# Optimization experiments

Hardware: AMD Instinct MI355X
Metric: run time of the kernel (lower is better)

Reference implementation:

```python
import jax, jax.numpy as jnp
import numpy as np

FEAT_DIM = 2048
HID = 256
N = 1024
NUM_CLASSES = 16
BN_EPS = 1e-5


def _batchnorm(x, gamma, beta):
    # training-mode BatchNorm1d: per-batch mean, biased variance
    m = x.mean(axis=0)
    v = x.var(axis=0)
    return gamma * (x - m) / jnp.sqrt(v + BN_EPS) + beta


def setup_inputs() -> dict:
    key = jax.random.key(0)
    ks = jax.random.split(key, 12)
    s1 = 1.0 / np.sqrt(FEAT_DIM)
    s2 = 1.0 / np.sqrt(HID)
    s3 = 1.0 / np.sqrt(2 * HID)
    return {
        "features": jax.random.normal(ks[0], (N, FEAT_DIM), dtype=jnp.float32),
        "labels": jax.random.randint(ks[1], (N,), 0, NUM_CLASSES, dtype=jnp.int32),
        # semantic disentangler
        "W1": jax.random.normal(ks[2], (FEAT_DIM, HID), dtype=jnp.float32) * s1,
        "b1": jnp.zeros((HID,), jnp.float32),
        "g1": jnp.ones((HID,), jnp.float32),
        "bt1": jnp.zeros((HID,), jnp.float32),
        "W2": jax.random.normal(ks[3], (HID, HID), dtype=jnp.float32) * s2,
        "b2": jnp.zeros((HID,), jnp.float32),
        "g2": jnp.ones((HID,), jnp.float32),
        "bt2": jnp.zeros((HID,), jnp.float32),
        # edge network: Linear(2H -> H), Linear(H -> 1)
        "We1": jax.random.normal(ks[4], (2 * HID, HID), dtype=jnp.float32) * s3,
        "bwe1": jnp.zeros((HID,), jnp.float32),
        "We2": jax.random.normal(ks[5], (HID, 1), dtype=jnp.float32) * s2,
        "bwe2": jnp.zeros((1,), jnp.float32),
    }


def reference(features, labels, W1, b1, g1, bt1, W2, b2, g2, bt2,
              We1, bwe1, We2, bwe2):
    # semantic disentangler: (Linear -> BN -> ReLU) x2
    h = jax.nn.relu(_batchnorm(features @ W1 + b1, g1, bt1))
    di = jax.nn.relu(_batchnorm(h @ W2 + b2, g2, bt2))  # [N, H]

    # EdgeNetwork all-pairs: Linear on concat([f_i, f_j]) splits into two GEMMs
    hi = di @ We1[:HID]   # [N, H] contribution of node i (first half of concat)
    hj = di @ We1[HID:]   # [N, H] contribution of node j (second half)
    pair = jax.nn.relu(hi[:, None, :] + hj[None, :, :] + bwe1)  # [N, N, H]
    logits = pair @ We2[:, 0] + bwe2[0]                          # [N, N]
    same_label = labels[:, None] == labels[None, :]
    off_diag = ~jnp.eye(N, dtype=bool)
    edge_weights = jnp.where(same_label & off_diag,
                             jax.nn.sigmoid(logits), 0.0)        # [N, N]

    # update_node_features: f_i + sum_j w_ij f_j / sum_j w_ij (if wsum > 0)
    weighted_sum = edge_weights @ di                 # [N, H] (w_ii == 0)
    wsum = edge_weights.sum(axis=1, keepdims=True)   # [N, 1]
    denom = jnp.where(wsum > 0, wsum, 1.0)
    updated = di + jnp.where(wsum > 0, weighted_sum / denom, 0.0)
    return updated
```

## Files before the change

kernel.cpp:

```cpp
#include <hip/hip_runtime.h>
#include <math.h>

#define N_PTS 1024
#define HID   256
#define FEAT  2048

typedef short bf16x8 __attribute__((ext_vector_type(8)));
typedef float f32x4  __attribute__((ext_vector_type(4)));

__device__ inline ushort f2bf(float f) {
    union { float f; unsigned u; } v; v.f = f;
    unsigned r = v.u + 0x7fff + ((v.u >> 16) & 1);
    return (ushort)(r >> 16);
}

__global__ __launch_bounds__(256) void prep(
    const float* __restrict__ features, const float* __restrict__ W1,
    const float* __restrict__ W2, const float* __restrict__ We1,
    ushort* __restrict__ Af, ushort* __restrict__ W1T,
    ushort* __restrict__ W2T, ushort* __restrict__ WeT)
{
    const int tid = threadIdx.x;
    int b = blockIdx.x;
    if (b < 512) {
        #pragma unroll
        for (int q = 0; q < 2; q++) {
            const size_t g = (size_t)b * 256 + tid + (size_t)q * 131072;
            float4 v0 = ((const float4*)features)[g * 2];
            float4 v1 = ((const float4*)features)[g * 2 + 1];
            bf16x8 o;
            o[0] = (short)f2bf(v0.x); o[1] = (short)f2bf(v0.y);
            o[2] = (short)f2bf(v0.z); o[3] = (short)f2bf(v0.w);
            o[4] = (short)f2bf(v1.x); o[5] = (short)f2bf(v1.y);
            o[6] = (short)f2bf(v1.z); o[7] = (short)f2bf(v1.w);
            ((bf16x8*)Af)[g] = o;
        }
        return;
    }
    __shared__ ushort Ts[64 * 72];
    const float* src; ushort* dst; int K;
    b -= 512;
    if (b < 128)      { src = W1;  dst = W1T; K = 2048; }
    else if (b < 144) { b -= 128; src = W2;  dst = W2T; K = 256; }
    else              { b -= 144; src = We1; dst = WeT; K = 512; }
    const int k0 = (b >> 2) * 64;
    const int n0 = (b & 3) * 64;
    #pragma unroll
    for (int p = 0; p < 4; p++) {
        const int c  = p * 256 + tid;
        const int r  = c >> 4;
        const int cq = c & 15;
        float4 v = *(const float4*)&src[(size_t)(k0 + r) * 256 + n0 + cq * 4];
        Ts[(cq * 4 + 0) * 72 + r] = f2bf(v.x);
        Ts[(cq * 4 + 1) * 72 + r] = f2bf(v.y);
        Ts[(cq * 4 + 2) * 72 + r] = f2bf(v.z);
        Ts[(cq * 4 + 3) * 72 + r] = f2bf(v.w);
    }
    __syncthreads();
    #pragma unroll
    for (int p = 0; p < 2; p++) {
        const int c    = p * 256 + tid;
        const int row  = c >> 3;
        const int col8 = c & 7;
        *(bf16x8*)&dst[(size_t)(n0 + row) * K + k0 + col8 * 8] =
            *(bf16x8*)&Ts[row * 72 + col8 * 8];
    }
}

__global__ __launch_bounds__(256) void gemm_bf(
    const ushort* __restrict__ A, const ushort* __restrict__ B,
    float* __restrict__ C, int lda, int ldb, int ldc, int kchunk)
{
    __shared__ ushort As[64 * 72];
    __shared__ ushort Bs[64 * 72];
    const int tid  = threadIdx.x;
    const int lane = tid & 63;
    const int wave = tid >> 6;
    const int wy = wave >> 1, wx = wave & 1;
    const int quad = lane >> 4, l16 = lane & 15;
    const int mBase = blockIdx.y * 64;
    const int nBase = blockIdx.x * 64;
    const int kBeg  = blockIdx.z * kchunk;

    f32x4 acc[2][2] = {};
    for (int ks = kBeg; ks < kBeg + kchunk; ks += 64) {
        #pragma unroll
        for (int p = 0; p < 2; p++) {
            const int c    = p * 256 + tid;
            const int row  = c >> 3;
            const int col8 = c & 7;
            *(bf16x8*)&As[row * 72 + col8 * 8] =
                *(const bf16x8*)&A[(size_t)(mBase + row) * lda + ks + col8 * 8];
            *(bf16x8*)&Bs[row * 72 + col8 * 8] =
                *(const bf16x8*)&B[(size_t)(nBase + row) * ldb + ks + col8 * 8];
        }
        __syncthreads();
        #pragma unroll
        for (int kt = 0; kt < 64; kt += 32) {
            bf16x8 af[2], bfr[2];
            #pragma unroll
            for (int mi = 0; mi < 2; mi++)
                af[mi] = *(bf16x8*)&As[(wy * 32 + mi * 16 + l16) * 72 + kt + quad * 8];
            #pragma unroll
            for (int ni = 0; ni < 2; ni++)
                bfr[ni] = *(bf16x8*)&Bs[(wx * 32 + ni * 16 + l16) * 72 + kt + quad * 8];
            #pragma unroll
            for (int mi = 0; mi < 2; mi++)
                #pragma unroll
                for (int ni = 0; ni < 2; ni++)
                    acc[mi][ni] = __builtin_amdgcn_mfma_f32_16x16x32_bf16(
                        af[mi], bfr[ni], acc[mi][ni], 0, 0, 0);
        }
        __syncthreads();
    }
    #pragma unroll
    for (int mi = 0; mi < 2; mi++)
        #pragma unroll
        for (int ni = 0; ni < 2; ni++)
            #pragma unroll
            for (int e = 0; e < 4; e++) {
                const int gm = mBase + wy * 32 + mi * 16 + quad * 4 + e;
                const int gn = nBase + wx * 32 + ni * 16 + l16;
                unsafeAtomicAdd(&C[(size_t)gm * ldc + gn], acc[mi][ni][e]);
            }
}

__global__ __launch_bounds__(256) void colstats(
    const float* __restrict__ X, float* __restrict__ sum,
    float* __restrict__ sq, int rowsPerBlock)
{
    const int c = threadIdx.x;
    const int r0 = blockIdx.x * rowsPerBlock;
    float s = 0.f, q = 0.f;
    for (int r = r0; r < r0 + rowsPerBlock; ++r) {
        float v = X[r * HID + c];
        s += v;
        q = fmaf(v, v, q);
    }
    unsafeAtomicAdd(&sum[c], s);
    unsafeAtomicAdd(&sq[c], q);
}

__global__ __launch_bounds__(256) void gemm2_fused(
    const float* __restrict__ A , const ushort* __restrict__ B ,
    float* __restrict__ C ,
    const float* __restrict__ sum1, const float* __restrict__ sq1,
    const float* __restrict__ g1, const float* __restrict__ bt1,
    float* __restrict__ sum2, float* __restrict__ sq2)
{
    __shared__ ushort As[64 * 72];
    __shared__ ushort Bs[64 * 72];
    __shared__ float sscale[HID];
    __shared__ float sshift[HID];
    __shared__ float csum[64];
    __shared__ float csq[64];
    const int tid  = threadIdx.x;
    const int lane = tid & 63;
    const int wave = tid >> 6;
    const int wy = wave >> 1, wx = wave & 1;
    const int quad = lane >> 4, l16 = lane & 15;
    const int mBase = blockIdx.y * 64;
    const int nBase = blockIdx.x * 64;

    {
        float m   = sum1[tid] * (1.f / 1024.f);
        float var = fmaf(-m, m, sq1[tid] * (1.f / 1024.f));
        float rstd = rsqrtf(var + 1e-5f);
        float sc = g1[tid] * rstd;
        sscale[tid] = sc;
        sshift[tid] = fmaf(-m, sc, bt1[tid]);
    }
    if (tid < 64) { csum[tid] = 0.f; csq[tid] = 0.f; }
    __syncthreads();

    f32x4 acc[2][2] = {};
    for (int ks = 0; ks < HID; ks += 64) {
        #pragma unroll
        for (int p = 0; p < 4; p++) {
            const int c  = p * 256 + tid;
            const int r  = c >> 4;
            const int cq = c & 15;
            const int k0 = ks + cq * 4;
            float4 av = *(const float4*)&A[(size_t)(mBase + r) * HID + k0];
            float v0 = fmaxf(fmaf(sscale[k0 + 0], av.x, sshift[k0 + 0]), 0.f);
            float v1 = fmaxf(fmaf(sscale[k0 + 1], av.y, sshift[k0 + 1]), 0.f);
            float v2 = fmaxf(fmaf(sscale[k0 + 2], av.z, sshift[k0 + 2]), 0.f);
            float v3 = fmaxf(fmaf(sscale[k0 + 3], av.w, sshift[k0 + 3]), 0.f);
            ushort4 ao;
            ao.x = f2bf(v0); ao.y = f2bf(v1); ao.z = f2bf(v2); ao.w = f2bf(v3);
            *(ushort4*)&As[r * 72 + cq * 4] = ao;
        }
        #pragma unroll
        for (int p = 0; p < 2; p++) {
            const int c    = p * 256 + tid;
            const int row  = c >> 3;
            const int col8 = c & 7;
            *(bf16x8*)&Bs[row * 72 + col8 * 8] =
                *(const bf16x8*)&B[(size_t)(nBase + row) * HID + ks + col8 * 8];
        }
        __syncthreads();
        #pragma unroll
        for (int kt = 0; kt < 64; kt += 32) {
            bf16x8 af[2], bfr[2];
            #pragma unroll
            for (int mi = 0; mi < 2; mi++)
                af[mi] = *(bf16x8*)&As[(wy * 32 + mi * 16 + l16) * 72 + kt + quad * 8];
            #pragma unroll
            for (int ni = 0; ni < 2; ni++)
                bfr[ni] = *(bf16x8*)&Bs[(wx * 32 + ni * 16 + l16) * 72 + kt + quad * 8];
            #pragma unroll
            for (int mi = 0; mi < 2; mi++)
                #pragma unroll
                for (int ni = 0; ni < 2; ni++)
                    acc[mi][ni] = __builtin_amdgcn_mfma_f32_16x16x32_bf16(
                        af[mi], bfr[ni], acc[mi][ni], 0, 0, 0);
        }
        __syncthreads();
    }

    float s[2] = {0.f, 0.f}, q[2] = {0.f, 0.f};
    #pragma unroll
    for (int mi = 0; mi < 2; mi++)
        #pragma unroll
        for (int ni = 0; ni < 2; ni++)
            #pragma unroll
            for (int e = 0; e < 4; e++) {
                const int gm = mBase + wy * 32 + mi * 16 + quad * 4 + e;
                const int gn = nBase + wx * 32 + ni * 16 + l16;
                float v = acc[mi][ni][e];
                C[(size_t)gm * HID + gn] = v;
                s[ni] += v;
                q[ni] = fmaf(v, v, q[ni]);
            }
    #pragma unroll
    for (int ni = 0; ni < 2; ni++) {
        float sv = s[ni], qv = q[ni];
        sv += __shfl_xor(sv, 16, 64); sv += __shfl_xor(sv, 32, 64);
        qv += __shfl_xor(qv, 16, 64); qv += __shfl_xor(qv, 32, 64);
        if (quad == 0) {
            atomicAdd(&csum[wx * 32 + ni * 16 + l16], sv);
            atomicAdd(&csq [wx * 32 + ni * 16 + l16], qv);
        }
    }
    __syncthreads();
    if (tid < 64) {
        unsafeAtomicAdd(&sum2[nBase + tid], csum[tid]);
        unsafeAtomicAdd(&sq2 [nBase + tid], csq[tid]);
    }
}

__global__ __launch_bounds__(256) void gemm_dual_bn(
    const float* __restrict__ A , const ushort* __restrict__ WeT,
    float* __restrict__ C1 , float* __restrict__ C2 ,
    const float* __restrict__ sum2, const float* __restrict__ sq2,
    const float* __restrict__ g2, const float* __restrict__ bt2,
    float* __restrict__ di)
{
    __shared__ ushort As[64 * 72];
    __shared__ ushort Bs[64 * 72];
    __shared__ float sscale[HID];
    __shared__ float sshift[HID];
    const int tid  = threadIdx.x;
    const int lane = tid & 63;
    const int wave = tid >> 6;
    const int wy = wave >> 1, wx = wave & 1;
    const int quad = lane >> 4, l16 = lane & 15;
    const int mBase = blockIdx.y * 64;
    const int nBase = blockIdx.x * 64;
    const int half  = blockIdx.z >> 2;
    const int ks    = (blockIdx.z & 3) * 64;
    float* C = half ? C2 : C1;
    const bool writeDi = (blockIdx.x == 0) && (half == 0);

    {
        float m   = sum2[tid] * (1.f / 1024.f);
        float var = fmaf(-m, m, sq2[tid] * (1.f / 1024.f));
        float rstd = rsqrtf(var + 1e-5f);
        float sc = g2[tid] * rstd;
        sscale[tid] = sc;
        sshift[tid] = fmaf(-m, sc, bt2[tid]);
    }
    __syncthreads();

    #pragma unroll
    for (int p = 0; p < 4; p++) {
        const int c  = p * 256 + tid;
        const int r  = c >> 4;
        const int cq = c & 15;
        const int k0 = ks + cq * 4;
        float4 av = *(const float4*)&A[(size_t)(mBase + r) * HID + k0];
        float v0 = fmaxf(fmaf(sscale[k0 + 0], av.x, sshift[k0 + 0]), 0.f);
        float v1 = fmaxf(fmaf(sscale[k0 + 1], av.y, sshift[k0 + 1]), 0.f);
        float v2 = fmaxf(fmaf(sscale[k0 + 2], av.z, sshift[k0 + 2]), 0.f);
        float v3 = fmaxf(fmaf(sscale[k0 + 3], av.w, sshift[k0 + 3]), 0.f);
        if (writeDi)
            *(float4*)&di[(size_t)(mBase + r) * HID + k0] =
                make_float4(v0, v1, v2, v3);
        ushort4 ao;
        ao.x = f2bf(v0); ao.y = f2bf(v1); ao.z = f2bf(v2); ao.w = f2bf(v3);
        *(ushort4*)&As[r * 72 + cq * 4] = ao;
    }
    #pragma unroll
    for (int p = 0; p < 2; p++) {
        const int c    = p * 256 + tid;
        const int row  = c >> 3;
        const int col8 = c & 7;
        *(bf16x8*)&Bs[row * 72 + col8 * 8] =
            *(const bf16x8*)&WeT[(size_t)(nBase + row) * 512 + half * 256 + ks + col8 * 8];
    }
    __syncthreads();

    f32x4 acc[2][2] = {};
    #pragma unroll
    for (int kt = 0; kt < 64; kt += 32) {
        bf16x8 af[2], bfr[2];
        #pragma unroll
        for (int mi = 0; mi < 2; mi++)
            af[mi] = *(bf16x8*)&As[(wy * 32 + mi * 16 + l16) * 72 + kt + quad * 8];
        #pragma unroll
        for (int ni = 0; ni < 2; ni++)
            bfr[ni] = *(bf16x8*)&Bs[(wx * 32 + ni * 16 + l16) * 72 + kt + quad * 8];
        #pragma unroll
        for (int mi = 0; mi < 2; mi++)
            #pragma unroll
            for (int ni = 0; ni < 2; ni++)
                acc[mi][ni] = __builtin_amdgcn_mfma_f32_16x16x32_bf16(
                    af[mi], bfr[ni], acc[mi][ni], 0, 0, 0);
    }
    #pragma unroll
    for (int mi = 0; mi < 2; mi++)
        #pragma unroll
        for (int ni = 0; ni < 2; ni++)
            #pragma unroll
            for (int e = 0; e < 4; e++) {
                const int gm = mBase + wy * 32 + mi * 16 + quad * 4 + e;
                const int gn = nBase + wx * 32 + ni * 16 + l16;
                unsafeAtomicAdd(&C[(size_t)gm * HID + gn], acc[mi][ni][e]);
            }
}

__global__ __launch_bounds__(256) void pair_update2(
    const float* __restrict__ di, const float* __restrict__ hi,
    const float* __restrict__ hj, const float* __restrict__ bwe1,
    const float* __restrict__ We2, const float* __restrict__ bwe2,
    const int* __restrict__ labels, float* __restrict__ out)
{
    __shared__ int   slab[N_PTS];
    __shared__ int   list[N_PTS];
    __shared__ int   cnt;
    __shared__ float sacc[16][HID];
    __shared__ float swsum[16];
    const int i   = blockIdx.x;
    const int tid = threadIdx.x;
    const int pid = tid >> 4;
    const int l16 = tid & 15;

    if (tid == 0) cnt = 0;
    for (int t = tid; t < N_PTS; t += 256) slab[t] = labels[t];
    __syncthreads();
    const int myLab = slab[i];
    for (int t = tid; t < N_PTS; t += 256)
        if (slab[t] == myLab && t != i) list[atomicAdd(&cnt, 1)] = t;
    __syncthreads();
    const int n = cnt;

    const float4* hip4 = (const float4*)(hi + (size_t)i * HID) + l16 * 4;
    const float4* bw4  = (const float4*)bwe1 + l16 * 4;
    const float4* w24  = (const float4*)We2  + l16 * 4;
    float4 hb[4], w2[4];
    #pragma unroll
    for (int s = 0; s < 4; s++) {
        float4 a = hip4[s], b = bw4[s];
        hb[s] = make_float4(a.x + b.x, a.y + b.y, a.z + b.z, a.w + b.w);
        w2[s] = w24[s];
    }
    const float b2 = bwe2[0];

    float4 acc[4] = {};
    float wloc = 0.f;
    const int rounds = (n + 15) >> 4;
    for (int r = 0; r < rounds; ++r) {
        const int idx = r * 16 + pid;
        const bool valid = idx < n;
        const int jj = valid ? list[idx] : i;
        const float4* hv4 = (const float4*)(hj + (size_t)jj * HID) + l16 * 4;
        float4 hv[4];
        #pragma unroll
        for (int s = 0; s < 4; s++) hv[s] = hv4[s];
        float p = 0.f;
        #pragma unroll
        for (int s = 0; s < 4; s++) {
            p = fmaf(fmaxf(hb[s].x + hv[s].x, 0.f), w2[s].x, p);
            p = fmaf(fmaxf(hb[s].y + hv[s].y, 0.f), w2[s].y, p);
            p = fmaf(fmaxf(hb[s].z + hv[s].z, 0.f), w2[s].z, p);
            p = fmaf(fmaxf(hb[s].w + hv[s].w, 0.f), w2[s].w, p);
        }
        p += __shfl_xor(p, 1, 64);
        p += __shfl_xor(p, 2, 64);
        p += __shfl_xor(p, 4, 64);
        p += __shfl_xor(p, 8, 64);
        const float w = valid ? 1.f / (1.f + expf(-(p + b2))) : 0.f;
        const float4* dv4 = (const float4*)(di + (size_t)jj * HID) + l16 * 4;
        #pragma unroll
        for (int s = 0; s < 4; s++) {
            float4 d = dv4[s];
            acc[s].x = fmaf(w, d.x, acc[s].x);
            acc[s].y = fmaf(w, d.y, acc[s].y);
            acc[s].z = fmaf(w, d.z, acc[s].z);
            acc[s].w = fmaf(w, d.w, acc[s].w);
        }
        if (l16 == 0) wloc += w;
    }
    #pragma unroll
    for (int s = 0; s < 4; s++)
        ((float4*)&sacc[pid][l16 * 16])[s] = acc[s];
    if (l16 == 0) swsum[pid] = wloc;
    __syncthreads();

    float at = 0.f;
    #pragma unroll
    for (int g = 0; g < 16; g++) at += sacc[g][tid];
    float wt = 0.f;
    #pragma unroll
    for (int g = 0; g < 16; g++) wt += swsum[g];
    const float dval = di[(size_t)i * HID + tid];
    out[(size_t)i * HID + tid] = dval + (wt > 0.f ? at / wt : 0.f);
}

extern "C" void kernel_launch(void* const* d_in, const int* in_sizes, int n_in,
                              void* d_out, int out_size, void* d_ws, size_t ws_size,
                              hipStream_t stream)
{
    const float* features = (const float*)d_in[0];
    const int*   labels   = (const int*)d_in[1];
    const float* W1   = (const float*)d_in[2];
    const float* g1   = (const float*)d_in[4];
    const float* bt1  = (const float*)d_in[5];
    const float* W2   = (const float*)d_in[6];
    const float* g2   = (const float*)d_in[8];
    const float* bt2  = (const float*)d_in[9];
    const float* We1  = (const float*)d_in[10];
    const float* bwe1 = (const float*)d_in[11];
    const float* We2  = (const float*)d_in[12];
    const float* bwe2 = (const float*)d_in[13];
    float* out = (float*)d_out;

    float* ws    = (float*)d_ws;
    float* x1    = ws;
    float* hi    = ws + 262144;
    float* hj    = ws + 524288;
    float* stats = ws + 786432;
    float* x2    = ws + 787456;
    float* di    = ws + 1049600;
    ushort* Af   = (ushort*)(ws + 1311744);
    ushort* W1T  = Af + 2097152;
    ushort* W2T  = W1T + 524288;
    ushort* WeT  = W2T + 65536;

    hipMemsetAsync(d_ws, 0, 787456 * sizeof(float), stream);

    dim3 blk(256);
    prep<<<688, blk, 0, stream>>>(features, W1, W2, We1, Af, W1T, W2T, WeT);
    gemm_bf<<<dim3(4, 16, 8), blk, 0, stream>>>(Af, W1T, x1,
                                                FEAT, FEAT, HID, 256);
    colstats<<<256, blk, 0, stream>>>(x1, stats, stats + 256, 4);
    gemm2_fused<<<dim3(4, 16, 1), blk, 0, stream>>>(x1, W2T, x2,
                                                    stats, stats + 256, g1, bt1,
                                                    stats + 512, stats + 768);
    gemm_dual_bn<<<dim3(4, 16, 8), blk, 0, stream>>>(x2, WeT, hi, hj,
                                                     stats + 512, stats + 768,
                                                     g2, bt2, di);
    pair_update2<<<N_PTS, blk, 0, stream>>>(di, hi, hj, bwe1, We2, bwe2,
                                            labels, out);
}
```

Before: 145.4 us.

## Replace atomic split-K accumulation with partial buffers and drop workspace memset

The first GEMM now writes each K-split's partial result to its own buffer with plain stores, and the column-stats kernel sums the eight partials before computing BN statistics. The edge GEMM loops over the full K inside each block instead of splitting K across blocks, so it too uses plain stores. The stats buffer is zeroed inside the prep kernel, which removes the separate memset. This trades float atomics and a memset launch for an extra 8 MB of partial-buffer traffic and fewer blocks in the edge GEMM.

New measurement: 138.4 us. 4.8% less time.

```diff
diff --git a/kernel.cpp b/kernel.cpp
--- a/kernel.cpp
+++ b/kernel.cpp
@@ -18,11 +18,14 @@
     const float* __restrict__ features, const float* __restrict__ W1,
     const float* __restrict__ W2, const float* __restrict__ We1,
     ushort* __restrict__ Af, ushort* __restrict__ W1T,
-    ushort* __restrict__ W2T, ushort* __restrict__ WeT)
+    ushort* __restrict__ W2T, ushort* __restrict__ WeT,
+    float* __restrict__ stats)
 {
     const int tid = threadIdx.x;
     int b = blockIdx.x;
     if (b < 512) {
+        if (b == 300)
+            ((float4*)stats)[tid] = make_float4(0.f, 0.f, 0.f, 0.f);
         #pragma unroll
         for (int q = 0; q < 2; q++) {
             const size_t g = (size_t)b * 256 + tid + (size_t)q * 131072;
@@ -67,9 +70,9 @@
     }
 }
 
-__global__ __launch_bounds__(256) void gemm_bf(
+__global__ __launch_bounds__(256) void gemm1p(
     const ushort* __restrict__ A, const ushort* __restrict__ B,
-    float* __restrict__ C, int lda, int ldb, int ldc, int kchunk)
+    float* __restrict__ Cp)
 {
     __shared__ ushort As[64 * 72];
     __shared__ ushort Bs[64 * 72];
@@ -80,19 +83,20 @@
     const int quad = lane >> 4, l16 = lane & 15;
     const int mBase = blockIdx.y * 64;
     const int nBase = blockIdx.x * 64;
-    const int kBeg  = blockIdx.z * kchunk;
+    const int kBeg  = blockIdx.z * 256;
+    float* C = Cp + (size_t)blockIdx.z * (N_PTS * HID);
 
     f32x4 acc[2][2] = {};
-    for (int ks = kBeg; ks < kBeg + kchunk; ks += 64) {
+    for (int ks = kBeg; ks < kBeg + 256; ks += 64) {
         #pragma unroll
         for (int p = 0; p < 2; p++) {
             const int c    = p * 256 + tid;
             const int row  = c >> 3;
             const int col8 = c & 7;
             *(bf16x8*)&As[row * 72 + col8 * 8] =
-                *(const bf16x8*)&A[(size_t)(mBase + row) * lda + ks + col8 * 8];
+                *(const bf16x8*)&A[(size_t)(mBase + row) * FEAT + ks + col8 * 8];
             *(bf16x8*)&Bs[row * 72 + col8 * 8] =
-                *(const bf16x8*)&B[(size_t)(nBase + row) * ldb + ks + col8 * 8];
+                *(const bf16x8*)&B[(size_t)(nBase + row) * FEAT + ks + col8 * 8];
         }
         __syncthreads();
         #pragma unroll
@@ -121,19 +125,23 @@
             for (int e = 0; e < 4; e++) {
                 const int gm = mBase + wy * 32 + mi * 16 + quad * 4 + e;
                 const int gn = nBase + wx * 32 + ni * 16 + l16;
-                unsafeAtomicAdd(&C[(size_t)gm * ldc + gn], acc[mi][ni][e]);
+                C[(size_t)gm * HID + gn] = acc[mi][ni][e];
             }
 }
 
-__global__ __launch_bounds__(256) void colstats(
-    const float* __restrict__ X, float* __restrict__ sum,
-    float* __restrict__ sq, int rowsPerBlock)
+__global__ __launch_bounds__(256) void reduce_stats(
+    const float* __restrict__ Xp, float* __restrict__ X,
+    float* __restrict__ sum, float* __restrict__ sq)
 {
     const int c = threadIdx.x;
-    const int r0 = blockIdx.x * rowsPerBlock;
+    const int r0 = blockIdx.x * 4;
     float s = 0.f, q = 0.f;
-    for (int r = r0; r < r0 + rowsPerBlock; ++r) {
-        float v = X[r * HID + c];
+    for (int r = r0; r < r0 + 4; ++r) {
+        float v = 0.f;
+        #pragma unroll
+        for (int z = 0; z < 8; z++)
+            v += Xp[(size_t)z * (N_PTS * HID) + r * HID + c];
+        X[r * HID + c] = v;
         s += v;
         q = fmaf(v, v, q);
     }
@@ -267,8 +275,7 @@
     const int quad = lane >> 4, l16 = lane & 15;
     const int mBase = blockIdx.y * 64;
     const int nBase = blockIdx.x * 64;
-    const int half  = blockIdx.z >> 2;
-    const int ks    = (blockIdx.z & 3) * 64;
+    const int half  = blockIdx.z;
     float* C = half ? C2 : C1;
     const bool writeDi = (blockIdx.x == 0) && (half == 0);
 
@@ -282,50 +289,52 @@
     }
     __syncthreads();
 
-    #pragma unroll
-    for (int p = 0; p < 4; p++) {
-        const int c  = p * 256 + tid;
-        const int r  = c >> 4;
-        const int cq = c & 15;
-        const int k0 = ks + cq * 4;
-        float4 av = *(const float4*)&A[(size_t)(mBase + r) * HID + k0];
-        float v0 = fmaxf(fmaf(sscale[k0 + 0], av.x, sshift[k0 + 0]), 0.f);
-        float v1 = fmaxf(fmaf(sscale[k0 + 1], av.y, sshift[k0 + 1]), 0.f);
-        float v2 = fmaxf(fmaf(sscale[k0 + 2], av.z, sshift[k0 + 2]), 0.f);
-        float v3 = fmaxf(fmaf(sscale[k0 + 3], av.w, sshift[k0 + 3]), 0.f);
-        if (writeDi)
-            *(float4*)&di[(size_t)(mBase + r) * HID + k0] =
-                make_float4(v0, v1, v2, v3);
-        ushort4 ao;
-        ao.x = f2bf(v0); ao.y = f2bf(v1); ao.z = f2bf(v2); ao.w = f2bf(v3);
-        *(ushort4*)&As[r * 72 + cq * 4] = ao;
-    }
-    #pragma unroll
-    for (int p = 0; p < 2; p++) {
-        const int c    = p * 256 + tid;
-        const int row  = c >> 3;
-        const int col8 = c & 7;
-        *(bf16x8*)&Bs[row * 72 + col8 * 8] =
-            *(const bf16x8*)&WeT[(size_t)(nBase + row) * 512 + half * 256 + ks + col8 * 8];
-    }
-    __syncthreads();
-
     f32x4 acc[2][2] = {};
-    #pragma unroll
-    for (int kt = 0; kt < 64; kt += 32) {
-        bf16x8 af[2], bfr[2];
-        #pragma unroll
-        for (int mi = 0; mi < 2; mi++)
-            af[mi] = *(bf16x8*)&As[(wy * 32 + mi * 16 + l16) * 72 + kt + quad * 8];
-        #pragma unroll
-        for (int ni = 0; ni < 2; ni++)
-            bfr[ni] = *(bf16x8*)&Bs[(wx * 32 + ni * 16 + l16) * 72 + kt + quad * 8];
-        #pragma unroll
-        for (int mi = 0; mi < 2; mi++)
+    for (int ks = 0; ks < HID; ks += 64) {
+        #pragma unroll
+        for (int p = 0; p < 4; p++) {
+            const int c  = p * 256 + tid;
+            const int r  = c >> 4;
+            const int cq = c & 15;
+            const int k0 = ks + cq * 4;
+            float4 av = *(const float4*)&A[(size_t)(mBase + r) * HID + k0];
+            float v0 = fmaxf(fmaf(sscale[k0 + 0], av.x, sshift[k0 + 0]), 0.f);
+            float v1 = fmaxf(fmaf(sscale[k0 + 1], av.y, sshift[k0 + 1]), 0.f);
+            float v2 = fmaxf(fmaf(sscale[k0 + 2], av.z, sshift[k0 + 2]), 0.f);
+            float v3 = fmaxf(fmaf(sscale[k0 + 3], av.w, sshift[k0 + 3]), 0.f);
+            if (writeDi)
+                *(float4*)&di[(size_t)(mBase + r) * HID + k0] =
+                    make_float4(v0, v1, v2, v3);
+            ushort4 ao;
+            ao.x = f2bf(v0); ao.y = f2bf(v1); ao.z = f2bf(v2); ao.w = f2bf(v3);
+            *(ushort4*)&As[r * 72 + cq * 4] = ao;
+        }
+        #pragma unroll
+        for (int p = 0; p < 2; p++) {
+            const int c    = p * 256 + tid;
+            const int row  = c >> 3;
+            const int col8 = c & 7;
+            *(bf16x8*)&Bs[row * 72 + col8 * 8] =
+                *(const bf16x8*)&WeT[(size_t)(nBase + row) * 512 + half * 256 + ks + col8 * 8];
+        }
+        __syncthreads();
+        #pragma unroll
+        for (int kt = 0; kt < 64; kt += 32) {
+            bf16x8 af[2], bfr[2];
+            #pragma unroll
+            for (int mi = 0; mi < 2; mi++)
+                af[mi] = *(bf16x8*)&As[(wy * 32 + mi * 16 + l16) * 72 + kt + quad * 8];
             #pragma unroll
             for (int ni = 0; ni < 2; ni++)
-                acc[mi][ni] = __builtin_amdgcn_mfma_f32_16x16x32_bf16(
-                    af[mi], bfr[ni], acc[mi][ni], 0, 0, 0);
+                bfr[ni] = *(bf16x8*)&Bs[(wx * 32 + ni * 16 + l16) * 72 + kt + quad * 8];
+            #pragma unroll
+            for (int mi = 0; mi < 2; mi++)
+                #pragma unroll
+                for (int ni = 0; ni < 2; ni++)
+                    acc[mi][ni] = __builtin_amdgcn_mfma_f32_16x16x32_bf16(
+                        af[mi], bfr[ni], acc[mi][ni], 0, 0, 0);
+        }
+        __syncthreads();
     }
     #pragma unroll
     for (int mi = 0; mi < 2; mi++)
@@ -335,7 +344,7 @@
             for (int e = 0; e < 4; e++) {
                 const int gm = mBase + wy * 32 + mi * 16 + quad * 4 + e;
                 const int gn = nBase + wx * 32 + ni * 16 + l16;
-                unsafeAtomicAdd(&C[(size_t)gm * HID + gn], acc[mi][ni][e]);
+                C[(size_t)gm * HID + gn] = acc[mi][ni][e];
             }
 }
 
@@ -452,22 +461,21 @@
     float* stats = ws + 786432;
     float* x2    = ws + 787456;
     float* di    = ws + 1049600;
-    ushort* Af   = (ushort*)(ws + 1311744);
+    float* x1p   = ws + 1311744;
+    ushort* Af   = (ushort*)(ws + 3408896);
     ushort* W1T  = Af + 2097152;
     ushort* W2T  = W1T + 524288;
     ushort* WeT  = W2T + 65536;
 
-    hipMemsetAsync(d_ws, 0, 787456 * sizeof(float), stream);
-
     dim3 blk(256);
-    prep<<<688, blk, 0, stream>>>(features, W1, W2, We1, Af, W1T, W2T, WeT);
-    gemm_bf<<<dim3(4, 16, 8), blk, 0, stream>>>(Af, W1T, x1,
-                                                FEAT, FEAT, HID, 256);
-    colstats<<<256, blk, 0, stream>>>(x1, stats, stats + 256, 4);
+    prep<<<688, blk, 0, stream>>>(features, W1, W2, We1, Af, W1T, W2T, WeT,
+                                  stats);
+    gemm1p<<<dim3(4, 16, 8), blk, 0, stream>>>(Af, W1T, x1p);
+    reduce_stats<<<256, blk, 0, stream>>>(x1p, x1, stats, stats + 256);
     gemm2_fused<<<dim3(4, 16, 1), blk, 0, stream>>>(x1, W2T, x2,
                                                     stats, stats + 256, g1, bt1,
                                                     stats + 512, stats + 768);
-    gemm_dual_bn<<<dim3(4, 16, 8), blk, 0, stream>>>(x2, WeT, hi, hj,
+    gemm_dual_bn<<<dim3(4, 16, 2), blk, 0, stream>>>(x2, WeT, hi, hj,
                                                      stats + 512, stats + 768,
                                                      g2, bt2, di);
     pair_update2<<<N_PTS, blk, 0, stream>>>(di, hi, hj, bwe1, We2, bwe2,
```
